# Performance work log

Measured on AMD Instinct MI355X. Metric: run time of the kernel, lower is better.

The kernel has to match this reference:

```python
import jax, jax.numpy as jnp
import numpy as np

NX, NH, NY, T = 128, 512, 1, 16384


def setup_inputs() -> dict:
    key = jax.random.key(0)
    ks = jax.random.split(key, 10)
    s = 0.01
    return {
        "x_t": jax.random.normal(ks[0], (T, 1), dtype=jnp.float32),
        "Wf": jax.random.normal(ks[1], (NH, NX), dtype=jnp.float32) * s,
        "Uf": jax.random.normal(ks[2], (NH, NH), dtype=jnp.float32) * s,
        "bf": jnp.zeros((NH,), dtype=jnp.float32),
        "Wi": jax.random.normal(ks[3], (NH, NX), dtype=jnp.float32) * s,
        "Ui": jax.random.normal(ks[4], (NH, NH), dtype=jnp.float32) * s,
        "bi": jnp.zeros((NH,), dtype=jnp.float32),
        "Wo": jax.random.normal(ks[5], (NH, NX), dtype=jnp.float32) * s,
        "Uo": jax.random.normal(ks[6], (NH, NH), dtype=jnp.float32) * s,
        "bo": jnp.zeros((NH,), dtype=jnp.float32),
        "Wc": jax.random.normal(ks[7], (NH, NX), dtype=jnp.float32) * s,
        "Uc": jax.random.normal(ks[8], (NH, NH), dtype=jnp.float32) * s,
        "bc": jnp.zeros((NH,), dtype=jnp.float32),
        "Ahy": jax.random.normal(ks[9], (NY, NH), dtype=jnp.float32) * s,
        "by": jnp.zeros((NY,), dtype=jnp.float32),
    }


def reference(x_t, Wf, Uf, bf, Wi, Ui, bi, Wo, Uo, bo, Wc, Uc, bc, Ahy, by):
    # x_t: (T, 1) univariate series; sliding windows of length Nx feed each step.
    Tlen = x_t.shape[0]
    Nx = Wf.shape[1]
    Nh = Wf.shape[0]
    steps = Tlen - Nx  # number of recurrent steps

    x = x_t[:, 0]  # (T,)
    idx = jnp.arange(steps)[:, None] + jnp.arange(Nx)[None, :]
    Xw = x[idx]  # (steps, Nx) sliding windows

    # Precompute input projections for all steps (batched GEMMs).
    xf = Xw @ Wf.T + bf  # (steps, Nh)
    xi = Xw @ Wi.T + bi
    xo = Xw @ Wo.T + bo
    xc = Xw @ Wc.T + bc

    def step(carry, inp):
        h, c = carry
        xf_t, xi_t, xo_t, xc_t = inp
        f = jax.nn.sigmoid(xf_t + Uf @ h)
        i = jax.nn.sigmoid(xi_t + Ui @ h)
        o = jax.nn.sigmoid(xo_t + Uo @ h)
        g = jnp.tanh(xc_t + Uc @ h)
        c = f * c + i * g
        h = o * jnp.tanh(c)
        mu = Ahy @ h + by  # (Ny,)
        return (h, c), mu

    init = (jnp.zeros((Nh,), x_t.dtype), jnp.zeros((Nh,), x_t.dtype))
    _, mu = jax.lax.scan(step, init, (xf, xi, xo, xc))
    return mu  # (steps, Ny) == (T-Nx, 1), matching torch's stack(...).unsqueeze(1)
```

## Files before the change

### kernel.cpp

```cpp
#include <hip/hip_runtime.h>

#define NHID 512
#define NXW  128
#define TLEN 16384
#define STEPS (TLEN - NXW)
#define G    32
#define B    512
#define RPW  16
#define RSLOTS 8

#define FOR4(M)  M(0) M(1) M(2) M(3)
#define FOR16(M) M(0) M(1) M(2) M(3) M(4) M(5) M(6) M(7) \
                 M(8) M(9) M(10) M(11) M(12) M(13) M(14) M(15)

__device__ __forceinline__ float sigmoid_f(float v) { return 1.f / (1.f + __expf(-v)); }
__device__ __forceinline__ float tanh_f(float v)    { return 1.f - 2.f / (1.f + __expf(2.f * v)); }

__launch_bounds__(B, 2)
__global__ void lstm_persistent(
    const float* x,
    const float* Wf, const float* Uf, const float* bf,
    const float* Wi, const float* Ui, const float* bi,
    const float* Wo, const float* Uo, const float* bo,
    const float* Wc, const float* Uc, const float* bc,
    unsigned long long* ring,
    float* h_hist)
{
    __shared__ float x_win[256];
    __shared__ __align__(16) float h_buf[8][64];
    __shared__ float partials[2][B];

    const int tid = threadIdx.x;
    const int g   = blockIdx.x;
    const int w   = tid >> 6;
    const int l   = tid & 63;
    const int q   = l >> 4;
    const int row = g * RPW + (l & 15);

    const float* Utab[4] = {Uf, Ui, Uo, Uc};
    const float* Wtab[4] = {Wf, Wi, Wo, Wc};
    const float* Btab[4] = {bf, bi, bo, bc};

    const float4* Up = (const float4*)(Utab[q] + (size_t)row * NHID + w * 64);
    #define DECLU(i) float4 u##i = Up[i];
    FOR16(DECLU)
    const float4* Wp = (const float4*)(Wtab[q] + row * NXW + w * 16);
    #define DECLW(i) float4 wv##i = Wp[i];
    FOR4(DECLW)
    #define PIN(r) asm volatile("" : "+v"(r.x), "+v"(r.y), "+v"(r.z), "+v"(r.w));
    #define PINU(i) PIN(u##i)
    FOR16(PINU)
    #define PINW(i) PIN(wv##i)
    FOR4(PINW)

    float bias = 0.f, c_prev = 0.f;
    if (w == 0) bias = Btab[q][row];

    h_buf[w][l] = 0.f;

    for (int t = 0; t < STEPS; ++t) {
        if ((t & 127) == 0) {
            __syncthreads();
            if (tid < 256) {
                int gi = t + tid;
                x_win[tid] = (gi < TLEN) ? x[gi] : 0.f;
            }
            __syncthreads();
        }

        float xacc = 0.f;
        {
            const int xb = (t & 127) + w * 16;
            #define XF(i) xacc += wv##i.x * x_win[xb + 4*i]     \
                                + wv##i.y * x_win[xb + 4*i + 1] \
                                + wv##i.z * x_win[xb + 4*i + 2] \
                                + wv##i.w * x_win[xb + 4*i + 3];
            FOR4(XF)
        }

        if (t > 0) {
            const unsigned long long* src =
                ring + ((size_t)((t - 1) & (RSLOTS - 1)) << 9) + (w * 64 + l);
            const unsigned want = (unsigned)(t - 1);
            unsigned long long vv; int guard = 0;
            do {
                vv = __hip_atomic_load(src, __ATOMIC_RELAXED, __HIP_MEMORY_SCOPE_AGENT);
            } while ((unsigned)(vv >> 32) != want && ++guard < (1 << 20));
            h_buf[w][l] = __uint_as_float((unsigned)vv);
        }

        float acc = xacc;
        const float4* hb4 = (const float4*)h_buf[w];
        #define UF(i) { float4 hv = hb4[i];                       \
                        acc += u##i.x * hv.x + u##i.y * hv.y      \
                             + u##i.z * hv.z + u##i.w * hv.w; }
        FOR16(UF)
        partials[t & 1][(w << 6) | l] = acc;
        __syncthreads();

        if (w == 0) {
            const float* p = partials[t & 1];
            float pre = acc + bias;
            #pragma unroll
            for (int s2 = 1; s2 < 8; ++s2) pre += p[s2 * 64 + l];
            float a = (l < 48) ? sigmoid_f(pre) : tanh_f(pre);
            float ai = __shfl(a, l + 16, 64);
            float ao = __shfl(a, l + 32, 64);
            float ag = __shfl(a, l + 48, 64);
            if (l < 16) {
                float c = a * c_prev + ai * ag;
                c_prev = c;
                float h = ao * tanh_f(c);
                unsigned long long pv =
                    ((unsigned long long)(unsigned)t << 32)
                    | (unsigned long long)__float_as_uint(h);
                __hip_atomic_store(
                    ring + ((size_t)(t & (RSLOTS - 1)) << 9) + row, pv,
                    __ATOMIC_RELAXED, __HIP_MEMORY_SCOPE_AGENT);
                h_hist[(size_t)t * NHID + row] = h;
            }
        }
    }
}

__global__ void mu_kernel(const float* __restrict__ h_hist,
                          const float* __restrict__ Ahy,
                          const float* __restrict__ by,
                          float* __restrict__ outp, int steps)
{
    int wave = threadIdx.x >> 6;
    int lane = threadIdx.x & 63;
    int t = blockIdx.x * 4 + wave;
    if (t >= steps) return;
    const float* h = h_hist + (size_t)t * NHID;
    float p = 0.f;
    #pragma unroll
    for (int e = 0; e < 8; e++)
        p += Ahy[e * 64 + lane] * h[e * 64 + lane];
    #pragma unroll
    for (int off = 32; off; off >>= 1) p += __shfl_down(p, off, 64);
    if (lane == 0) outp[t] = p + by[0];
}

extern "C" void kernel_launch(void* const* d_in, const int* in_sizes, int n_in,
                              void* d_out, int out_size, void* d_ws, size_t ws_size,
                              hipStream_t stream)
{
    const float* x  = (const float*)d_in[0];
    const float* Wf = (const float*)d_in[1];
    const float* Uf = (const float*)d_in[2];
    const float* bf = (const float*)d_in[3];
    const float* Wi = (const float*)d_in[4];
    const float* Ui = (const float*)d_in[5];
    const float* bi = (const float*)d_in[6];
    const float* Wo = (const float*)d_in[7];
    const float* Uo = (const float*)d_in[8];
    const float* bo = (const float*)d_in[9];
    const float* Wc = (const float*)d_in[10];
    const float* Uc = (const float*)d_in[11];
    const float* bc = (const float*)d_in[12];
    const float* Ahy = (const float*)d_in[13];
    const float* by  = (const float*)d_in[14];

    unsigned long long* ring = (unsigned long long*)d_ws;
    float* h_hist = (float*)((char*)d_ws + RSLOTS * NHID * 8);

    lstm_persistent<<<G, B, 0, stream>>>(x, Wf, Uf, bf, Wi, Ui, bi,
                                         Wo, Uo, bo, Wc, Uc, bc, ring, h_hist);
    int muBlocks = (STEPS + 3) / 4;
    mu_kernel<<<muBlocks, 256, 0, stream>>>(h_hist, Ahy, by, (float*)d_out, STEPS);
}
```

Measured before the change: 25.57 ms.

## Spread persistent blocks across XCDs and poll ring via sc0 L2 loads

Launches 256 blocks and keeps only every eighth one active, so that, assuming round-robin block placement across XCDs, the 32 working blocks land on one XCD and can share its L2. The inter-block h exchange now uses inline-asm sc0 loads and stores that are meant to be served from that shared L2. If a value does not show up after a bounded number of polls, the reader falls back to agent-scope atomics. The change also issues the ring load before the input projection to hide its latency, splits accumulations into independent chains for more ILP, and shrinks the ring to 4 slots. It relies on an undocumented block-to-XCD mapping, and it writes each ring entry twice, once per store path.

```diff
diff --git a/kernel.cpp b/kernel.cpp
--- a/kernel.cpp
+++ b/kernel.cpp
@@ -4,10 +4,10 @@
 #define NXW  128
 #define TLEN 16384
 #define STEPS (TLEN - NXW)
-#define G    32
+#define GRID 256
 #define B    512
 #define RPW  16
-#define RSLOTS 8
+#define RSLOTS 4
 
 #define FOR4(M)  M(0) M(1) M(2) M(3)
 #define FOR16(M) M(0) M(1) M(2) M(3) M(4) M(5) M(6) M(7) \
@@ -15,6 +15,16 @@
 
 __device__ __forceinline__ float sigmoid_f(float v) { return 1.f / (1.f + __expf(-v)); }
 __device__ __forceinline__ float tanh_f(float v)    { return 1.f - 2.f / (1.f + __expf(2.f * v)); }
+
+__device__ __forceinline__ unsigned long long ld_ring_l2(const unsigned long long* p) {
+    unsigned long long v;
+    asm volatile("global_load_dwordx2 %0, %1, off sc0\n\ts_waitcnt vmcnt(0)"
+                 : "=v"(v) : "v"(p) : "memory");
+    return v;
+}
+__device__ __forceinline__ void st_ring_l2(unsigned long long* p, unsigned long long v) {
+    asm volatile("global_store_dwordx2 %0, %1, off sc0" :: "v"(p), "v"(v) : "memory");
+}
 
 __launch_bounds__(B, 2)
 __global__ void lstm_persistent(
@@ -26,12 +36,14 @@
     unsigned long long* ring,
     float* h_hist)
 {
+    if (blockIdx.x & 7) return;
+    const int g = blockIdx.x >> 3;
+
     __shared__ float x_win[256];
     __shared__ __align__(16) float h_buf[8][64];
     __shared__ float partials[2][B];
 
     const int tid = threadIdx.x;
-    const int g   = blockIdx.x;
     const int w   = tid >> 6;
     const int l   = tid & 63;
     const int q   = l >> 4;
@@ -58,6 +70,8 @@
 
     h_buf[w][l] = 0.f;
 
+    bool lfast = true;
+
     for (int t = 0; t < STEPS; ++t) {
         if ((t & 127) == 0) {
             __syncthreads();
@@ -68,41 +82,61 @@
             __syncthreads();
         }
 
-        float xacc = 0.f;
+        const unsigned want = (unsigned)(t - 1);
+        const unsigned long long* src =
+            ring + ((size_t)((t - 1) & (RSLOTS - 1)) << 9) + (w * 64 + l);
+        unsigned long long vv = 0;
+        if (t > 0)
+            vv = lfast ? ld_ring_l2(src)
+                       : __hip_atomic_load(src, __ATOMIC_RELAXED, __HIP_MEMORY_SCOPE_AGENT);
+
+        float xa0 = 0.f, xa1 = 0.f;
         {
             const int xb = (t & 127) + w * 16;
-            #define XF(i) xacc += wv##i.x * x_win[xb + 4*i]     \
+            #define XF(i, A) A += wv##i.x * x_win[xb + 4*i]     \
                                 + wv##i.y * x_win[xb + 4*i + 1] \
                                 + wv##i.z * x_win[xb + 4*i + 2] \
                                 + wv##i.w * x_win[xb + 4*i + 3];
-            FOR4(XF)
-        }
+            XF(0, xa0) XF(1, xa1) XF(2, xa0) XF(3, xa1)
+        }
+        const float xacc = xa0 + xa1;
 
         if (t > 0) {
-            const unsigned long long* src =
-                ring + ((size_t)((t - 1) & (RSLOTS - 1)) << 9) + (w * 64 + l);
-            const unsigned want = (unsigned)(t - 1);
-            unsigned long long vv; int guard = 0;
-            do {
-                vv = __hip_atomic_load(src, __ATOMIC_RELAXED, __HIP_MEMORY_SCOPE_AGENT);
-            } while ((unsigned)(vv >> 32) != want && ++guard < (1 << 20));
+            if (lfast) {
+                int guard = 0;
+                while ((unsigned)(vv >> 32) != want) {
+                    if (++guard == 8192) { lfast = false; break; }
+                    vv = ld_ring_l2(src);
+                }
+            }
+            if (!lfast) {
+                while ((unsigned)(vv >> 32) != want)
+                    vv = __hip_atomic_load(src, __ATOMIC_RELAXED, __HIP_MEMORY_SCOPE_AGENT);
+            }
             h_buf[w][l] = __uint_as_float((unsigned)vv);
         }
 
-        float acc = xacc;
+        float ac0 = xacc, ac1 = 0.f, ac2 = 0.f, ac3 = 0.f;
         const float4* hb4 = (const float4*)h_buf[w];
-        #define UF(i) { float4 hv = hb4[i];                       \
-                        acc += u##i.x * hv.x + u##i.y * hv.y      \
-                             + u##i.z * hv.z + u##i.w * hv.w; }
-        FOR16(UF)
-        partials[t & 1][(w << 6) | l] = acc;
+        #define UF(i, A) { float4 hv = hb4[i];                    \
+                           A += u##i.x * hv.x + u##i.y * hv.y     \
+                              + u##i.z * hv.z + u##i.w * hv.w; }
+        UF(0,  ac0) UF(1,  ac1) UF(2,  ac2) UF(3,  ac3)
+        UF(4,  ac0) UF(5,  ac1) UF(6,  ac2) UF(7,  ac3)
+        UF(8,  ac0) UF(9,  ac1) UF(10, ac2) UF(11, ac3)
+        UF(12, ac0) UF(13, ac1) UF(14, ac2) UF(15, ac3)
+        const float acc = (ac0 + ac1) + (ac2 + ac3);
+
+        partials[t & 1][tid] = acc;
         __syncthreads();
 
         if (w == 0) {
             const float* p = partials[t & 1];
-            float pre = acc + bias;
-            #pragma unroll
-            for (int s2 = 1; s2 < 8; ++s2) pre += p[s2 * 64 + l];
+            float r0 = p[64  + l] + p[128 + l];
+            float r1 = p[192 + l] + p[256 + l];
+            float r2 = p[320 + l] + p[384 + l];
+            float r3 = p[448 + l];
+            float pre = ((acc + bias) + r0) + ((r1 + r2) + r3);
             float a = (l < 48) ? sigmoid_f(pre) : tanh_f(pre);
             float ai = __shfl(a, l + 16, 64);
             float ao = __shfl(a, l + 32, 64);
@@ -114,8 +148,10 @@
                 unsigned long long pv =
                     ((unsigned long long)(unsigned)t << 32)
                     | (unsigned long long)__float_as_uint(h);
-                __hip_atomic_store(
-                    ring + ((size_t)(t & (RSLOTS - 1)) << 9) + row, pv,
+                unsigned long long* dst =
+                    ring + ((size_t)(t & (RSLOTS - 1)) << 9) + row;
+                st_ring_l2(dst, pv);
+                __hip_atomic_store(dst, pv,
                     __ATOMIC_RELAXED, __HIP_MEMORY_SCOPE_AGENT);
                 h_hist[(size_t)t * NHID + row] = h;
             }
@@ -165,8 +201,8 @@
     unsigned long long* ring = (unsigned long long*)d_ws;
     float* h_hist = (float*)((char*)d_ws + RSLOTS * NHID * 8);
 
-    lstm_persistent<<<G, B, 0, stream>>>(x, Wf, Uf, bf, Wi, Ui, bi,
-                                         Wo, Uo, bo, Wc, Uc, bc, ring, h_hist);
+    lstm_persistent<<<GRID, B, 0, stream>>>(x, Wf, Uf, bf, Wi, Ui, bi,
+                                            Wo, Uo, bo, Wc, Uc, bc, ring, h_hist);
     int muBlocks = (STEPS + 3) / 4;
     mu_kernel<<<muBlocks, 256, 0, stream>>>(h_hist, Ahy, by, (float*)d_out, STEPS);
 }
```

New measurement: 38.00 ms. 48.6% more time.

## Overlap ring polling with x projection, ring-buffer x window, split accumulators

Applied to the files above, without the earlier changes.

Turns the x window into a 512-entry circular buffer with a 128-element mirrored tail. Wave 7 refills it asynchronously every 128 steps, which removes the two block-wide barriers per refill. The first ring load is issued before the input-projection dot product so its latency overlaps that arithmetic. Polling now keeps three loads in flight with s_sleep between them. The dot products and the partial reduction use multiple independent accumulators to shorten dependency chains. This risks races on the x window refill, because wave 7 writes ahead without a barrier and relies on the per-step syncthreads for ordering.

```diff
diff --git a/kernel.cpp b/kernel.cpp
--- a/kernel.cpp
+++ b/kernel.cpp
@@ -8,6 +8,7 @@
 #define B    512
 #define RPW  16
 #define RSLOTS 8
+#define XWIN 640
 
 #define FOR4(M)  M(0) M(1) M(2) M(3)
 #define FOR16(M) M(0) M(1) M(2) M(3) M(4) M(5) M(6) M(7) \
@@ -15,6 +16,9 @@
 
 __device__ __forceinline__ float sigmoid_f(float v) { return 1.f / (1.f + __expf(-v)); }
 __device__ __forceinline__ float tanh_f(float v)    { return 1.f - 2.f / (1.f + __expf(2.f * v)); }
+
+#define AL(p) __hip_atomic_load((p), __ATOMIC_RELAXED, __HIP_MEMORY_SCOPE_AGENT)
+#define SLP() asm volatile("s_sleep 4")
 
 __launch_bounds__(B, 2)
 __global__ void lstm_persistent(
@@ -26,7 +30,7 @@
     unsigned long long* ring,
     float* h_hist)
 {
-    __shared__ float x_win[256];
+    __shared__ float x_win[XWIN];
     __shared__ __align__(16) float h_buf[8][64];
     __shared__ float partials[2][B];
 
@@ -58,57 +62,89 @@
 
     h_buf[w][l] = 0.f;
 
+    {
+        float v = x[tid];
+        x_win[tid] = v;
+        if (tid < XWIN - 512) x_win[512 + tid] = v;
+    }
+    __syncthreads();
+
     for (int t = 0; t < STEPS; ++t) {
-        if ((t & 127) == 0) {
-            __syncthreads();
-            if (tid < 256) {
-                int gi = t + tid;
-                x_win[tid] = (gi < TLEN) ? x[gi] : 0.f;
+        if (((t & 127) == 0) && w == 7) {
+            int j = t + 256 + (l << 1);
+            #pragma unroll
+            for (int k2 = 0; k2 < 2; ++k2) {
+                int jj = j + k2;
+                float v = (jj < TLEN) ? x[jj] : 0.f;
+                int s = jj & 511;
+                x_win[s] = v;
+                if (s < XWIN - 512) x_win[512 + s] = v;
             }
-            __syncthreads();
-        }
-
-        float xacc = 0.f;
+        }
+
+        const unsigned want = (unsigned)(t - 1);
+        const unsigned long long* src =
+            ring + ((size_t)((t - 1) & (RSLOTS - 1)) << 9) + (w * 64 + l);
+        unsigned long long a = 0;
+        if (t > 0) a = AL(src);
+
+        float xa0 = 0.f, xa1 = 0.f;
         {
-            const int xb = (t & 127) + w * 16;
-            #define XF(i) xacc += wv##i.x * x_win[xb + 4*i]     \
+            const int xb = (t & 511) + w * 16;
+            #define XF(i, A) A += wv##i.x * x_win[xb + 4*i]     \
                                 + wv##i.y * x_win[xb + 4*i + 1] \
                                 + wv##i.z * x_win[xb + 4*i + 2] \
                                 + wv##i.w * x_win[xb + 4*i + 3];
-            FOR4(XF)
-        }
+            XF(0, xa0) XF(1, xa1) XF(2, xa0) XF(3, xa1)
+        }
+        const float xacc = xa0 + xa1;
 
         if (t > 0) {
-            const unsigned long long* src =
-                ring + ((size_t)((t - 1) & (RSLOTS - 1)) << 9) + (w * 64 + l);
-            const unsigned want = (unsigned)(t - 1);
-            unsigned long long vv; int guard = 0;
-            do {
-                vv = __hip_atomic_load(src, __ATOMIC_RELAXED, __HIP_MEMORY_SCOPE_AGENT);
-            } while ((unsigned)(vv >> 32) != want && ++guard < (1 << 20));
-            h_buf[w][l] = __uint_as_float((unsigned)vv);
-        }
-
-        float acc = xacc;
+            if ((unsigned)(a >> 32) != want) {
+                unsigned long long b0 = AL(src); SLP();
+                unsigned long long b1 = AL(src); SLP();
+                unsigned long long b2 = AL(src);
+                int guard = 1 << 20;
+                for (;;) {
+                    if ((unsigned)(b0 >> 32) == want) { a = b0; break; }
+                    b0 = AL(src);
+                    if ((unsigned)(b1 >> 32) == want) { a = b1; break; }
+                    b1 = AL(src);
+                    if ((unsigned)(b2 >> 32) == want) { a = b2; break; }
+                    b2 = AL(src);
+                    if (--guard == 0) { a = b2; break; }
+                }
+            }
+            h_buf[w][l] = __uint_as_float((unsigned)a);
+        }
+
+        float ac0 = xacc, ac1 = 0.f, ac2 = 0.f, ac3 = 0.f;
         const float4* hb4 = (const float4*)h_buf[w];
-        #define UF(i) { float4 hv = hb4[i];                       \
-                        acc += u##i.x * hv.x + u##i.y * hv.y      \
-                             + u##i.z * hv.z + u##i.w * hv.w; }
-        FOR16(UF)
-        partials[t & 1][(w << 6) | l] = acc;
+        #define UF(i, A) { float4 hv = hb4[i];                    \
+                           A += u##i.x * hv.x + u##i.y * hv.y     \
+                              + u##i.z * hv.z + u##i.w * hv.w; }
+        UF(0,  ac0) UF(1,  ac1) UF(2,  ac2) UF(3,  ac3)
+        UF(4,  ac0) UF(5,  ac1) UF(6,  ac2) UF(7,  ac3)
+        UF(8,  ac0) UF(9,  ac1) UF(10, ac2) UF(11, ac3)
+        UF(12, ac0) UF(13, ac1) UF(14, ac2) UF(15, ac3)
+        const float acc = (ac0 + ac1) + (ac2 + ac3);
+
+        partials[t & 1][tid] = acc;
         __syncthreads();
 
         if (w == 0) {
             const float* p = partials[t & 1];
-            float pre = acc + bias;
-            #pragma unroll
-            for (int s2 = 1; s2 < 8; ++s2) pre += p[s2 * 64 + l];
-            float a = (l < 48) ? sigmoid_f(pre) : tanh_f(pre);
-            float ai = __shfl(a, l + 16, 64);
-            float ao = __shfl(a, l + 32, 64);
-            float ag = __shfl(a, l + 48, 64);
+            float r0 = p[64  + l] + p[128 + l];
+            float r1 = p[192 + l] + p[256 + l];
+            float r2 = p[320 + l] + p[384 + l];
+            float r3 = p[448 + l];
+            float pre = ((acc + bias) + r0) + ((r1 + r2) + r3);
+            float a2 = (l < 48) ? sigmoid_f(pre) : tanh_f(pre);
+            float ai = __shfl(a2, l + 16, 64);
+            float ao = __shfl(a2, l + 32, 64);
+            float ag = __shfl(a2, l + 48, 64);
             if (l < 16) {
-                float c = a * c_prev + ai * ag;
+                float c = a2 * c_prev + ai * ag;
                 c_prev = c;
                 float h = ao * tanh_f(c);
                 unsigned long long pv =
```

New measurement: 28.11 ms. +10.0%, slower.
